# Performance work log

Measured on AMD Instinct MI355X. Metric: run time of the kernel, lower is better.

Reference implementation:

```python
import jax, jax.numpy as jnp
import numpy as np

D_MODEL = 96
D_INNER = 192        # expand_factor * d_model
D_STATE = 16
DT_RANK = 6          # ceil(d_model / 16)
D_CONV = 4
N_LAYERS = 2
EPS = 1e-5


def conv3d(x, w, b=None, padding=((0, 0), (0, 0), (0, 0)), groups=1):
    # x: (N, C, L, H, W), w: (O, C//groups, kL, kH, kW)
    y = jax.lax.conv_general_dilated(
        x, w, window_strides=(1, 1, 1), padding=padding,
        dimension_numbers=('NCDHW', 'OIDHW', 'NCDHW'),
        feature_group_count=groups)
    return y if b is None else y + b[None, :, None, None, None]


def rmsnorm(x, w):
    # faithful to source: mean of squares over the LAST dim (W)
    return x * jax.lax.rsqrt(jnp.mean(x * x, axis=-1, keepdims=True) + EPS) * w


def mamba_block(x, p):
    # x: (N, d_model, L, H, W)
    L = x.shape[2]
    xz = conv3d(x, p['in_proj_w'], padding=((0, 0), (1, 1), (1, 1)))
    xi, z = xz[:, :D_INNER], xz[:, D_INNER:]
    # causal depthwise temporal conv: pad d_conv-1, crop to L
    xi = conv3d(xi, p['conv1d_w'], p['conv1d_b'],
                padding=((D_CONV - 1, D_CONV - 1), (0, 0), (0, 0)),
                groups=D_INNER)[:, :, :L]
    xi = jax.nn.silu(xi)
    # --- SSM (selective scan, pscan path) ---
    A = -jnp.exp(p['A_log'])                                   # (K, S)
    dbc = conv3d(xi, p['x_proj_w'])                            # (N, dt_rank+2S, L, H, W)
    delta = jax.nn.softplus(conv3d(dbc[:, :DT_RANK], p['dt_proj_w'], p['dt_proj_b']))  # (N, K, L, H, W)
    B = jnp.moveaxis(dbc[:, DT_RANK:DT_RANK + D_STATE], 1, -1)  # (N, L, H, W, S)
    C = dbc[:, DT_RANK + D_STATE:]                              # (N, S, L, H, W)
    deltaA = jnp.exp(delta[..., None] * A[None, :, None, None, None, :])  # (N,K,L,H,W,S)
    BX = delta[..., None] * B[:, None] * xi[..., None]                    # (N,K,L,H,W,S)

    def op(e1, e2):
        a1, b1 = e1
        a2, b2 = e2
        return a1 * a2, a2 * b1 + b2

    _, hs = jax.lax.associative_scan(op, (deltaA, BX), axis=2)  # scan over L
    y = jnp.einsum('nklhws,nslhw->nklhw', hs, C) + p['D'][None, :, None, None, None] * xi
    out = y * jax.nn.silu(z)
    return conv3d(out, p['out_proj_w'])


def _forward(x, in_proj_w, conv1d_w, conv1d_b, x_proj_w, dt_proj_w,
             dt_proj_b, A_log, D, out_proj_w, norm_w):
    for l in range(N_LAYERS):
        p = dict(in_proj_w=in_proj_w[l], conv1d_w=conv1d_w[l], conv1d_b=conv1d_b[l],
                 x_proj_w=x_proj_w[l], dt_proj_w=dt_proj_w[l], dt_proj_b=dt_proj_b[l],
                 A_log=A_log[l], D=D[l], out_proj_w=out_proj_w[l], norm_w=norm_w[l])
        x = mamba_block(rmsnorm(x, p['norm_w']), p) + x   # ResidualBlock
        x = x[:, :, 0:1]                                   # Mamba.forward keeps t=0 only
    return x


def setup_inputs() -> dict:
    key = jax.random.key(0)
    ks = jax.random.split(key, 12)
    Lk = N_LAYERS
    x = jax.random.normal(ks[0], (2, D_MODEL, 8, 24, 24), dtype=jnp.float32)
    in_proj_w = jax.random.normal(ks[1], (Lk, 2 * D_INNER, D_MODEL, 1, 3, 3), jnp.float32) * (D_MODEL * 9) ** -0.5
    conv1d_w = jax.random.normal(ks[2], (Lk, D_INNER, 1, D_CONV, 1, 1), jnp.float32) * D_CONV ** -0.5
    conv1d_b = jax.random.normal(ks[3], (Lk, D_INNER), jnp.float32) * 0.02
    x_proj_w = jax.random.normal(ks[4], (Lk, DT_RANK + 2 * D_STATE, D_INNER, 1, 1, 1), jnp.float32) * D_INNER ** -0.5
    dt_std = DT_RANK ** -0.5
    dt_proj_w = jax.random.uniform(ks[5], (Lk, D_INNER, DT_RANK, 1, 1, 1), jnp.float32, -dt_std, dt_std)
    # dt bias init: inv softplus of dt ~ LogUniform(dt_min, dt_max)
    dt = jnp.exp(jax.random.uniform(ks[6], (Lk, D_INNER), jnp.float32)
                 * (np.log(0.1) - np.log(0.001)) + np.log(0.001))
    dt = jnp.clip(dt, 1e-4, None)
    dt_proj_b = dt + jnp.log(-jnp.expm1(-dt))
    A_log = jnp.log(jnp.tile(jnp.arange(1, D_STATE + 1, dtype=jnp.float32), (Lk, D_INNER, 1)))
    D = jnp.ones((Lk, D_INNER), jnp.float32)
    out_proj_w = jax.random.normal(ks[7], (Lk, D_MODEL, D_INNER, 1, 1, 1), jnp.float32) * D_INNER ** -0.5
    norm_w = jnp.ones((Lk, 1, D_MODEL, 1, 1, 1), jnp.float32)
    return {'x': x, 'in_proj_w': in_proj_w, 'conv1d_w': conv1d_w, 'conv1d_b': conv1d_b,
            'x_proj_w': x_proj_w, 'dt_proj_w': dt_proj_w, 'dt_proj_b': dt_proj_b,
            'A_log': A_log, 'D': D, 'out_proj_w': out_proj_w, 'norm_w': norm_w}


def reference(x, in_proj_w, conv1d_w, conv1d_b, x_proj_w, dt_proj_w,
              dt_proj_b, A_log, D, out_proj_w, norm_w):
    return _forward(x, in_proj_w, conv1d_w, conv1d_b, x_proj_w, dt_proj_w,
                    dt_proj_b, A_log, D, out_proj_w, norm_w)
```

## Files before the change

### kernel.cpp

```cpp
#include <hip/hip_runtime.h>
#include <math.h>

#define NB   2
#define CM   96
#define CI   192
#define CO   384
#define HP   24
#define WP   24
#define PX   576
#define DTR  6
#define NDBC 38
#define CSPLIT 4
#define CCH  24

__device__ __forceinline__ float siluf(float x){ return x / (1.f + expf(-x)); }
__device__ __forceinline__ float softplusf(float x){ return x > 20.f ? x : log1pf(expf(x)); }

#define NW_IN (2*CO*CM*9)
#define WQ_L  (CM*2*CO*4)
#define WR_L  (CM*CO)
#define WP_L  (CI*CM)
__global__ void prep_k(const float* __restrict__ ipw, const float* __restrict__ opw,
                       float* __restrict__ wQ, float* __restrict__ wR, float* __restrict__ wpT){
    int idx = blockIdx.x*256 + threadIdx.x;
    if (idx < NW_IN){
        int l = idx / (CO*CM*9);
        int r = idx % (CO*CM*9);
        int o = r / (CM*9);
        int r2 = r % (CM*9);
        int c = r2 / 9;
        int k = r2 % 9;
        float v = ipw[idx];
        if (k < 8) wQ[l*WQ_L + ((c*2 + (k>>2))*CO + o)*4 + (k&3)] = v;
        else       wR[l*WR_L + c*CO + o] = v;
    } else {
        int j = idx - NW_IN;
        if (j < 2*CI*CM){
            int l = j / (CI*CM);
            int r = j % (CI*CM);
            int c = r / CM;
            int m = r % CM;
            wpT[l*WP_L + c*CM + m] = opw[(l*CM + m)*CI + c];
        }
    }
}

__global__ __launch_bounds__(256) void conv_k(
    const float* __restrict__ x, long nStr, long cStr,
    const float* __restrict__ nw,
    const float* __restrict__ wQ, const float* __restrict__ wR,
    float* __restrict__ acc)
{
    __shared__ float hs[CCH][3][26];
    __shared__ float scl[CCH][3];
    int bx = blockIdx.x;
    int og = blockIdx.y;
    int cs = blockIdx.z;
    int n = bx / HP, hh = bx % HP;
    int tid = threadIdx.x;
    int c0 = cs*CCH;

    if (tid < CCH*3){
        int c = tid/3, j = tid%3;
        int row = hh + j - 1;
        float s = 0.f;
        if (row >= 0 && row < HP){
            const float* xp = x + (long)n*nStr + (long)(c0+c)*cStr + row*WP;
            #pragma unroll
            for (int w = 0; w < WP; w++){ float v = xp[w]; s += v*v; }
            s = rsqrtf(s*(1.0f/WP) + 1e-5f) * nw[c0+c];
        }
        scl[c][j] = s;
    }
    __syncthreads();

    for (int idx = tid; idx < CCH*3*26; idx += 256){
        int c = idx/78; int rem = idx%78; int j = rem/26; int wc = rem%26;
        int row = hh + j - 1;
        float v = 0.f;
        if (row >= 0 && row < HP && wc >= 1 && wc <= WP)
            v = x[(long)n*nStr + (long)(c0+c)*cStr + row*WP + (wc-1)] * scl[c][j];
        hs[c][j][wc] = v;
    }
    __syncthreads();

    int ol = tid & 63;
    int o  = og*64 + ol;
    int w0 = (tid >> 6) * 6;
    float acc6[6] = {0,0,0,0,0,0};
    const float4* wq4 = (const float4*)wQ;

    for (int c = 0; c < CCH; c++){
        int cg = c0 + c;
        float4 wa = wq4[(cg*2+0)*CO + o];
        float4 wb = wq4[(cg*2+1)*CO + o];
        float w8 = wR[cg*CO + o];
        float r0[8], r1[8], r2[8];
        #pragma unroll
        for (int i = 0; i < 8; i++){
            r0[i] = hs[c][0][w0+i]; r1[i] = hs[c][1][w0+i]; r2[i] = hs[c][2][w0+i];
        }
        #pragma unroll
        for (int p = 0; p < 6; p++){
            acc6[p] += wa.x*r0[p]   + wa.y*r0[p+1] + wa.z*r0[p+2]
                     + wa.w*r1[p]   + wb.x*r1[p+1] + wb.y*r1[p+2]
                     + wb.z*r2[p]   + wb.w*r2[p+1] + w8  *r2[p+2];
        }
    }

    float* ap = acc + ((long)(cs*NB + n)*PX + hh*WP + w0)*CO + o;
    #pragma unroll
    for (int p = 0; p < 6; p++) ap[p*CO] = acc6[p];
}

__global__ __launch_bounds__(256) void ssmproj_k(
    const float* __restrict__ acc,
    const float* __restrict__ c1w, const float* __restrict__ c1b,
    const float* __restrict__ xpw, const float* __restrict__ dtw,
    const float* __restrict__ dtb, const float* __restrict__ Dp,
    const float* __restrict__ wpT,
    const float* __restrict__ xres, long nStrR, long cStrR,
    float* __restrict__ dst)
{
    __shared__ float gl[4][CI];
    int wave = threadIdx.x >> 6, lane = threadIdx.x & 63;
    int p0 = blockIdx.x*4;
    int p  = p0 + wave;
    int n  = p / PX, px = p % PX;

    float xi[3], sz[3];
    #pragma unroll
    for (int t = 0; t < 3; t++){
        int c = lane + 64*t;
        float xr = 0.f, zr = 0.f;
        #pragma unroll
        for (int q = 0; q < CSPLIT; q++){
            const float* ap = acc + ((long)(q*NB + n)*PX + px)*CO;
            xr += ap[c]; zr += ap[CI + c];
        }
        xi[t] = siluf(xr*c1w[c*4 + 3] + c1b[c]);
        sz[t] = siluf(zr);
    }

    float dbc[NDBC];
    #pragma unroll
    for (int j = 0; j < NDBC; j++){
        float s = 0.f;
        #pragma unroll
        for (int t = 0; t < 3; t++) s += xi[t]*xpw[j*CI + lane + 64*t];
        dbc[j] = s;
    }
    #pragma unroll
    for (int step = 1; step < 64; step <<= 1){
        #pragma unroll
        for (int j = 0; j < NDBC; j++) dbc[j] += __shfl_xor(dbc[j], step, 64);
    }
    float BC = 0.f;
    #pragma unroll
    for (int s = 0; s < 16; s++) BC += dbc[6+s]*dbc[22+s];

    #pragma unroll
    for (int t = 0; t < 3; t++){
        int c = lane + 64*t;
        float dl = dtb[c];
        #pragma unroll
        for (int r = 0; r < DTR; r++) dl += dbc[r]*dtw[c*DTR + r];
        dl = softplusf(dl);
        gl[wave][c] = xi[t]*(dl*BC + Dp[c])*sz[t];
    }
    __syncthreads();

    for (int idx = threadIdx.x; idx < 4*CM; idx += 256){
        int pl = idx / CM, m = idx % CM;
        int pp = p0 + pl;
        int nn = pp / PX, ppx = pp % PX;
        const float* g = gl[pl];
        float s0 = 0.f, s1 = 0.f, s2 = 0.f, s3 = 0.f;
        for (int c = 0; c < CI; c += 4){
            s0 += g[c+0]*wpT[(c+0)*CM + m];
            s1 += g[c+1]*wpT[(c+1)*CM + m];
            s2 += g[c+2]*wpT[(c+2)*CM + m];
            s3 += g[c+3]*wpT[(c+3)*CM + m];
        }
        float s = (s0+s1) + (s2+s3);
        s += xres[(long)nn*nStrR + (long)m*cStrR + ppx];
        dst[(nn*CM + m)*PX + ppx] = s;
    }
}

extern "C" void kernel_launch(void* const* d_in, const int* in_sizes, int n_in,
                              void* d_out, int out_size, void* d_ws, size_t ws_size,
                              hipStream_t stream) {
    const float* x_in = (const float*)d_in[0];
    const float* ipw  = (const float*)d_in[1];
    const float* c1w  = (const float*)d_in[2];
    const float* c1b  = (const float*)d_in[3];
    const float* xpw  = (const float*)d_in[4];
    const float* dtw  = (const float*)d_in[5];
    const float* dtb  = (const float*)d_in[6];
    const float* Dp   = (const float*)d_in[8];
    const float* opw  = (const float*)d_in[9];
    const float* nw   = (const float*)d_in[10];

    float* ws  = (float*)d_ws;
    float* wQ  = ws;
    float* wR  = wQ  + 2*WQ_L;
    float* wpT = wR  + 2*WR_L;
    float* acc = wpT + 2*WP_L;
    float* x1  = acc + (long)CSPLIT*NB*PX*CO;

    prep_k<<<(NW_IN + 2*CI*CM + 255)/256, 256, 0, stream>>>(ipw, opw, wQ, wR, wpT);

    conv_k<<<dim3(NB*HP, 6, CSPLIT), 256, 0, stream>>>(
        x_in, 96L*8*PX, 8L*PX, nw, wQ, wR, acc);
    ssmproj_k<<<NB*PX/4, 256, 0, stream>>>(
        acc, c1w, c1b, xpw, dtw, dtb, Dp, wpT,
        x_in, 96L*8*PX, 8L*PX, x1);

    conv_k<<<dim3(NB*HP, 6, CSPLIT), 256, 0, stream>>>(
        x1, 96L*PX, (long)PX, nw + CM, wQ + WQ_L, wR + WR_L, acc);
    ssmproj_k<<<NB*PX/4, 256, 0, stream>>>(
        acc, c1w + CI*4, c1b + CI, xpw + NDBC*CI, dtw + CI*DTR, dtb + CI, Dp + CI, wpT + WP_L,
        x1, 96L*PX, (long)PX, (float*)d_out);
}
```

Baseline: 166.3 us.

## Store conv weights as bf16 and compute two output rows per block

The in-projection conv weights are converted to bf16 once in the prep kernel and packed as one uint4 per (channel, output). Each conv block now computes two output rows that share a four-row halo tile. This halves weight traffic and reuses every weight load across two rows, with half as many blocks. In exchange, bf16 rounding of the weights adds numerical error, and grid parallelism and occupancy drop.

```diff
diff --git a/kernel.cpp b/kernel.cpp
--- a/kernel.cpp
+++ b/kernel.cpp
@@ -12,16 +12,24 @@
 #define NDBC 38
 #define CSPLIT 4
 #define CCH  24
+#define ROWS 2
 
 __device__ __forceinline__ float siluf(float x){ return x / (1.f + expf(-x)); }
 __device__ __forceinline__ float softplusf(float x){ return x > 20.f ? x : log1pf(expf(x)); }
+__device__ __forceinline__ unsigned short f2bf(float f){
+    unsigned u = __float_as_uint(f);
+    return (unsigned short)((u + 0x7fffu + ((u >> 16) & 1u)) >> 16);
+}
+__device__ __forceinline__ float bflo(unsigned u){ return __uint_as_float(u << 16); }
+__device__ __forceinline__ float bfhi(unsigned u){ return __uint_as_float(u & 0xffff0000u); }
 
 #define NW_IN (2*CO*CM*9)
-#define WQ_L  (CM*2*CO*4)
-#define WR_L  (CM*CO)
-#define WP_L  (CI*CM)
+#define WQB_L (CM*CO*8)
+#define WRB_L (CM*CO)
+#define WPT_L (CI*CM)
 __global__ void prep_k(const float* __restrict__ ipw, const float* __restrict__ opw,
-                       float* __restrict__ wQ, float* __restrict__ wR, float* __restrict__ wpT){
+                       unsigned short* __restrict__ wQb, unsigned short* __restrict__ wRb,
+                       float* __restrict__ wpT){
     int idx = blockIdx.x*256 + threadIdx.x;
     if (idx < NW_IN){
         int l = idx / (CO*CM*9);
@@ -30,9 +38,9 @@
         int r2 = r % (CM*9);
         int c = r2 / 9;
         int k = r2 % 9;
-        float v = ipw[idx];
-        if (k < 8) wQ[l*WQ_L + ((c*2 + (k>>2))*CO + o)*4 + (k&3)] = v;
-        else       wR[l*WR_L + c*CO + o] = v;
+        unsigned short v = f2bf(ipw[idx]);
+        if (k < 8) wQb[(long)l*WQB_L + ((c*CO + o)<<3) + k] = v;
+        else       wRb[(long)l*WRB_L + c*CO + o] = v;
     } else {
         int j = idx - NW_IN;
         if (j < 2*CI*CM){
@@ -40,7 +48,7 @@
             int r = j % (CI*CM);
             int c = r / CM;
             int m = r % CM;
-            wpT[l*WP_L + c*CM + m] = opw[(l*CM + m)*CI + c];
+            wpT[l*WPT_L + c*CM + m] = opw[(l*CM + m)*CI + c];
         }
     }
 }
@@ -48,21 +56,22 @@
 __global__ __launch_bounds__(256) void conv_k(
     const float* __restrict__ x, long nStr, long cStr,
     const float* __restrict__ nw,
-    const float* __restrict__ wQ, const float* __restrict__ wR,
+    const unsigned short* __restrict__ wQb, const unsigned short* __restrict__ wRb,
     float* __restrict__ acc)
 {
-    __shared__ float hs[CCH][3][26];
-    __shared__ float scl[CCH][3];
+    __shared__ float hs[CCH][ROWS+2][26];
+    __shared__ float scl[CCH][ROWS+2];
     int bx = blockIdx.x;
     int og = blockIdx.y;
     int cs = blockIdx.z;
-    int n = bx / HP, hh = bx % HP;
+    int n  = bx / (HP/ROWS);
+    int r0 = (bx % (HP/ROWS))*ROWS;
     int tid = threadIdx.x;
     int c0 = cs*CCH;
 
-    if (tid < CCH*3){
-        int c = tid/3, j = tid%3;
-        int row = hh + j - 1;
+    if (tid < CCH*(ROWS+2)){
+        int c = tid/(ROWS+2), j = tid%(ROWS+2);
+        int row = r0 + j - 1;
         float s = 0.f;
         if (row >= 0 && row < HP){
             const float* xp = x + (long)n*nStr + (long)(c0+c)*cStr + row*WP;
@@ -74,9 +83,9 @@
     }
     __syncthreads();
 
-    for (int idx = tid; idx < CCH*3*26; idx += 256){
-        int c = idx/78; int rem = idx%78; int j = rem/26; int wc = rem%26;
-        int row = hh + j - 1;
+    for (int idx = tid; idx < CCH*(ROWS+2)*26; idx += 256){
+        int c = idx/((ROWS+2)*26); int rem = idx%((ROWS+2)*26); int j = rem/26; int wc = rem%26;
+        int row = r0 + j - 1;
         float v = 0.f;
         if (row >= 0 && row < HP && wc >= 1 && wc <= WP)
             v = x[(long)n*nStr + (long)(c0+c)*cStr + row*WP + (wc-1)] * scl[c][j];
@@ -86,31 +95,40 @@
 
     int ol = tid & 63;
     int o  = og*64 + ol;
-    int w0 = (tid >> 6) * 6;
-    float acc6[6] = {0,0,0,0,0,0};
-    const float4* wq4 = (const float4*)wQ;
+    int x0 = (tid >> 6) * 6;
+    float a0[6] = {0,0,0,0,0,0};
+    float a1[6] = {0,0,0,0,0,0};
+    const uint4* wq4 = (const uint4*)wQb;
 
     for (int c = 0; c < CCH; c++){
         int cg = c0 + c;
-        float4 wa = wq4[(cg*2+0)*CO + o];
-        float4 wb = wq4[(cg*2+1)*CO + o];
-        float w8 = wR[cg*CO + o];
-        float r0[8], r1[8], r2[8];
+        uint4 wv = wq4[cg*CO + o];
+        float w0 = bflo(wv.x), w1 = bfhi(wv.x);
+        float w2 = bflo(wv.y), w3 = bfhi(wv.y);
+        float w4 = bflo(wv.z), w5 = bfhi(wv.z);
+        float w6 = bflo(wv.w), w7 = bfhi(wv.w);
+        float w8 = bflo((unsigned)wRb[cg*CO + o]);
+        float r0v[8], r1v[8], r2v[8], r3v[8];
         #pragma unroll
         for (int i = 0; i < 8; i++){
-            r0[i] = hs[c][0][w0+i]; r1[i] = hs[c][1][w0+i]; r2[i] = hs[c][2][w0+i];
+            r0v[i] = hs[c][0][x0+i]; r1v[i] = hs[c][1][x0+i];
+            r2v[i] = hs[c][2][x0+i]; r3v[i] = hs[c][3][x0+i];
         }
         #pragma unroll
         for (int p = 0; p < 6; p++){
-            acc6[p] += wa.x*r0[p]   + wa.y*r0[p+1] + wa.z*r0[p+2]
-                     + wa.w*r1[p]   + wb.x*r1[p+1] + wb.y*r1[p+2]
-                     + wb.z*r2[p]   + wb.w*r2[p+1] + w8  *r2[p+2];
-        }
-    }
-
-    float* ap = acc + ((long)(cs*NB + n)*PX + hh*WP + w0)*CO + o;
-    #pragma unroll
-    for (int p = 0; p < 6; p++) ap[p*CO] = acc6[p];
+            a0[p] += w0*r0v[p] + w1*r0v[p+1] + w2*r0v[p+2]
+                   + w3*r1v[p] + w4*r1v[p+1] + w5*r1v[p+2]
+                   + w6*r2v[p] + w7*r2v[p+1] + w8*r2v[p+2];
+            a1[p] += w0*r1v[p] + w1*r1v[p+1] + w2*r1v[p+2]
+                   + w3*r2v[p] + w4*r2v[p+1] + w5*r2v[p+2]
+                   + w6*r3v[p] + w7*r3v[p+1] + w8*r3v[p+2];
+        }
+    }
+
+    float* ap0 = acc + ((long)(cs*NB + n)*PX + r0*WP + x0)*CO + o;
+    float* ap1 = ap0 + (long)WP*CO;
+    #pragma unroll
+    for (int p = 0; p < 6; p++){ ap0[p*CO] = a0[p]; ap1[p*CO] = a1[p]; }
 }
 
 __global__ __launch_bounds__(256) void ssmproj_k(
@@ -202,24 +220,24 @@
     const float* opw  = (const float*)d_in[9];
     const float* nw   = (const float*)d_in[10];
 
-    float* ws  = (float*)d_ws;
-    float* wQ  = ws;
-    float* wR  = wQ  + 2*WQ_L;
-    float* wpT = wR  + 2*WR_L;
-    float* acc = wpT + 2*WP_L;
+    char* ws = (char*)d_ws;
+    unsigned short* wQb = (unsigned short*)ws;
+    unsigned short* wRb = wQb + 2*WQB_L;
+    float* wpT = (float*)(wRb + 2*WRB_L);
+    float* acc = wpT + 2*WPT_L;
     float* x1  = acc + (long)CSPLIT*NB*PX*CO;
 
-    prep_k<<<(NW_IN + 2*CI*CM + 255)/256, 256, 0, stream>>>(ipw, opw, wQ, wR, wpT);
-
-    conv_k<<<dim3(NB*HP, 6, CSPLIT), 256, 0, stream>>>(
-        x_in, 96L*8*PX, 8L*PX, nw, wQ, wR, acc);
+    prep_k<<<(NW_IN + 2*CI*CM + 255)/256, 256, 0, stream>>>(ipw, opw, wQb, wRb, wpT);
+
+    conv_k<<<dim3(NB*(HP/ROWS), 6, CSPLIT), 256, 0, stream>>>(
+        x_in, 96L*8*PX, 8L*PX, nw, wQb, wRb, acc);
     ssmproj_k<<<NB*PX/4, 256, 0, stream>>>(
         acc, c1w, c1b, xpw, dtw, dtb, Dp, wpT,
         x_in, 96L*8*PX, 8L*PX, x1);
 
-    conv_k<<<dim3(NB*HP, 6, CSPLIT), 256, 0, stream>>>(
-        x1, 96L*PX, (long)PX, nw + CM, wQ + WQ_L, wR + WR_L, acc);
+    conv_k<<<dim3(NB*(HP/ROWS), 6, CSPLIT), 256, 0, stream>>>(
+        x1, 96L*PX, (long)PX, nw + CM, wQb + WQB_L, wRb + WRB_L, acc);
     ssmproj_k<<<NB*PX/4, 256, 0, stream>>>(
-        acc, c1w + CI*4, c1b + CI, xpw + NDBC*CI, dtw + CI*DTR, dtb + CI, Dp + CI, wpT + WP_L,
+        acc, c1w + CI*4, c1b + CI, xpw + NDBC*CI, dtw + CI*DTR, dtb + CI, Dp + CI, wpT + WPT_L,
         x1, 96L*PX, (long)PX, (float*)d_out);
 }
```

Result: slower. 173.3 us (+4.2%).
